# Kernel optimization log

Measured on AMD Instinct MI355X. Metric: run time of the kernel, lower is better.

## Reference

```python
import jax, jax.numpy as jnp
import numpy as np

D_LINK = 64   # link_state_dim
D_PATH = 64   # path_state_dim
T = 3
MAX_LEN = 8   # max hops per path (max(seqs)+1)
R_UNITS = 256


def _glorot(k, shape):
    lim = np.sqrt(6.0 / (shape[0] + shape[-1])).astype(np.float32)
    return jax.random.uniform(k, shape, minval=-lim, maxval=lim, dtype=jnp.float32)


def setup_inputs() -> dict:
    key = jax.random.key(0)
    ks = jax.random.split(key, 16)
    n_links, n_paths, L = 50000, 100000, MAX_LEN
    capacities = jax.random.uniform(ks[0], (n_links,), dtype=jnp.float32) + 0.5
    traffic = jax.random.uniform(ks[1], (n_paths,), dtype=jnp.float32)
    # every path traverses L links; entries sorted by path id (tf.segment_sum assumption)
    paths = jnp.repeat(jnp.arange(n_paths, dtype=jnp.int32), L)
    seqs = jnp.tile(jnp.arange(L, dtype=jnp.int32), n_paths)
    links = jax.random.randint(ks[2], (n_paths * L,), 0, n_links, dtype=jnp.int32)
    return dict(
        capacities=capacities, traffic=traffic, links=links, paths=paths, seqs=seqs,
        Wx_p=_glorot(ks[3], (D_LINK, 3 * D_PATH)), Wh_p=_glorot(ks[4], (D_PATH, 3 * D_PATH)),
        b_p=jnp.zeros((3 * D_PATH,), jnp.float32),
        Wx_e=_glorot(ks[5], (D_PATH, 3 * D_LINK)), Wh_e=_glorot(ks[6], (D_LINK, 3 * D_LINK)),
        b_e=jnp.zeros((3 * D_LINK,), jnp.float32),
        W_r1=_glorot(ks[7], (D_PATH, R_UNITS)), b_r1=jnp.zeros((R_UNITS,), jnp.float32),
        W_r2=_glorot(ks[8], (R_UNITS, R_UNITS)), b_r2=jnp.zeros((R_UNITS,), jnp.float32),
        W_f=_glorot(ks[9], (D_PATH + R_UNITS, 1)), b_f=jnp.zeros((1,), jnp.float32),
        n_links=n_links, n_paths=n_paths,
    )


def gru_cell(x, h, Wx, Wh, b):
    # Keras GRUCell (reset_after=False), gate order z, r, h
    gx = x @ Wx + b
    gh = h @ Wh
    u = h.shape[-1]
    z = jax.nn.sigmoid(gx[..., :u] + gh[..., :u])
    r = jax.nn.sigmoid(gx[..., u:2 * u] + gh[..., u:2 * u])
    hc = jnp.tanh(gx[..., 2 * u:] + r * gh[..., 2 * u:])
    return z * h + (1.0 - z) * hc


def routenet_fwd(capacities, traffic, links, paths, seqs,
                 Wx_p, Wh_p, b_p, Wx_e, Wh_e, b_e,
                 W_r1, b_r1, W_r2, b_r2, W_f, b_f, n_links, n_paths):
    link_state = jnp.concatenate(
        [capacities[:, None], jnp.zeros((n_links, D_LINK - 1), capacities.dtype)], axis=1)
    path_state = jnp.concatenate(
        [traffic[:, None], jnp.zeros((n_paths, D_PATH - 1), traffic.dtype)], axis=1)
    lens = jax.ops.segment_sum(jnp.ones_like(paths), paths, num_segments=n_paths)  # [P]

    for _ in range(T):
        h_ = link_state[links]                                        # [E, D_LINK]
        link_inputs = jnp.zeros((n_paths, MAX_LEN, D_LINK), h_.dtype).at[paths, seqs].set(h_)

        def step(h, inp):
            xt, t = inp
            hn = gru_cell(xt, h, Wx_p, Wh_p, b_p)
            valid = (t < lens)[:, None]
            hn = jnp.where(valid, hn, h)          # dynamic_rnn copies state past seq len
            out = jnp.where(valid, hn, 0.0)       # and emits zeros there
            return hn, out

        path_state, outs = jax.lax.scan(
            step, path_state,
            (jnp.transpose(link_inputs, (1, 0, 2)), jnp.arange(MAX_LEN)))
        m = jnp.transpose(outs, (1, 0, 2))[paths, seqs]               # [E, D_PATH]
        m = jax.ops.segment_sum(m, links, num_segments=n_links)      # [n_links, D_PATH]
        link_state = gru_cell(m, link_state, Wx_e, Wh_e, b_e)

    r = jax.nn.selu(path_state @ W_r1 + b_r1)
    r = jax.nn.selu(r @ W_r2 + b_r2)          # dropout inactive (training=False)
    o = jnp.concatenate([r, path_state], axis=1) @ W_f + b_f
    return o


def reference(capacities, traffic, links, paths, seqs,
              Wx_p, Wh_p, b_p, Wx_e, Wh_e, b_e,
              W_r1, b_r1, W_r2, b_r2, W_f, b_f, n_links, n_paths):
    return routenet_fwd(capacities, traffic, links, paths, seqs,
                        Wx_p, Wh_p, b_p, Wx_e, Wh_e, b_e,
                        W_r1, b_r1, W_r2, b_r2, W_f, b_f, n_links, n_paths)
```

## Files before the change

kernel.cpp:

```cpp
#include <hip/hip_runtime.h>

typedef unsigned short ushort_t;
typedef unsigned int   uint_t;
typedef short bf16x8 __attribute__((ext_vector_type(8)));
typedef float f32x4  __attribute__((ext_vector_type(4)));

#define MFMA16(a,b,c) __builtin_amdgcn_mfma_f32_16x16x32_bf16((a),(b),(c),0,0,0)

static __device__ __forceinline__ float bf2f(ushort_t b) {
  union { uint_t u; float f; } v; v.u = ((uint_t)b) << 16; return v.f;
}
static __device__ __forceinline__ ushort_t f2bf(float f) {
  union { float f; uint_t u; } v; v.f = f;
  uint_t r = v.u + 0x7fffu + ((v.u >> 16) & 1u);
  return (ushort_t)(r >> 16);
}
static __device__ __forceinline__ float frcp(float x) { return __builtin_amdgcn_rcpf(x); }
static __device__ __forceinline__ float sigm(float x) { return frcp(1.0f + __expf(-x)); }
static __device__ __forceinline__ float ftanh(float x) { return 1.0f - 2.0f * frcp(1.0f + __expf(2.0f * x)); }
static __device__ __forceinline__ float selu_f(float x) {
  float e = 1.6732632423543772f * (__expf(x) - 1.0f);
  return 1.0507009873554805f * (x > 0.0f ? x : e);
}
static __device__ __forceinline__ bf16x8 pack8(float4 a, float4 b) {
  bf16x8 r;
  r[0] = (short)f2bf(a.x); r[1] = (short)f2bf(a.y); r[2] = (short)f2bf(a.z); r[3] = (short)f2bf(a.w);
  r[4] = (short)f2bf(b.x); r[5] = (short)f2bf(b.y); r[6] = (short)f2bf(b.z); r[7] = (short)f2bf(b.w);
  return r;
}
static __device__ __forceinline__ void split8(float4 a, float4 b, bf16x8& hi, bf16x8& lo) {
  hi = pack8(a, b);
  float4 ra, rb;
  ra.x = a.x - bf2f((ushort_t)hi[0]); ra.y = a.y - bf2f((ushort_t)hi[1]);
  ra.z = a.z - bf2f((ushort_t)hi[2]); ra.w = a.w - bf2f((ushort_t)hi[3]);
  rb.x = b.x - bf2f((ushort_t)hi[4]); rb.y = b.y - bf2f((ushort_t)hi[5]);
  rb.z = b.z - bf2f((ushort_t)hi[6]); rb.w = b.w - bf2f((ushort_t)hi[7]);
  lo = pack8(ra, rb);
}

#define GFRAG(ptr, f) (*(const bf16x8*)&(ptr)[(((f) * 64 + lane)) * 8])
#define LFRAG(arr, f) (*(const bf16x8*)&(arr)[(((f) * 64 + lane)) * 8])

__global__ void detect_dtype(const uint_t* __restrict__ caps, int* __restrict__ flag) {
  int lane = threadIdx.x;
  uint_t d = caps[lane];
  uint_t lo = d & 0xFFFFu, hi = d >> 16;
  bool isbf = (lo >= 0x3F00u && lo <= 0x3FC0u) && (hi >= 0x3F00u && hi <= 0x3FC0u);
  unsigned long long m = __ballot(isbf);
  if (lane == 0) *flag = (__popcll(m) >= 48) ? 1 : 0;
}

#define NARR 14
struct ConvDesc {
  const void* src[NARR];
  float*      dst[NARR];
  int         n[NARR];
  int         blk0[NARR + 1];
};
__global__ void conv_all(ConvDesc d, const int* __restrict__ flag) {
  int isbf = *flag;
  int b = blockIdx.x;
  int a = 0;
  while (a + 1 < NARR && b >= d.blk0[a + 1]) ++a;
  int idx = (b - d.blk0[a]) * 256 + threadIdx.x;
  if (idx >= d.n[a]) return;
  d.dst[a][idx] = isbf ? bf2f(((const ushort_t*)d.src[a])[idx])
                       : ((const float*)d.src[a])[idx];
}

__global__ void pack_split(const float* __restrict__ srcA, const float* __restrict__ srcB,
                           int srcN, int colOff, int splitK, int nCk, int NT,
                           ushort_t* __restrict__ dstH, ushort_t* __restrict__ dstL) {
  int i = blockIdx.x * 256 + threadIdx.x;
  int total = nCk * NT * 512;
  if (i >= total) return;
  int j = i & 7;
  int lane = (i >> 3) & 63;
  int f = i >> 9;
  int c = f / NT, nt = f - c * NT;
  int k = c * 32 + ((lane >> 4) << 3) + j;
  int n = colOff + nt * 16 + (lane & 15);
  float v = (k < splitK) ? srcA[k * srcN + n] : srcB[(k - splitK) * srcN + n];
  ushort_t hi = f2bf(v);
  dstH[i] = hi;
  dstL[i] = f2bf(v - bf2f(hi));
}

__global__ void init_states(const float* __restrict__ caps, const float* __restrict__ traffic,
                            ushort_t* __restrict__ linkHL,
                            float* __restrict__ path_state, int n_links, int n_paths) {
  long i = (long)blockIdx.x * 256 + threadIdx.x;
  long total = (long)(n_links + n_paths) * 64;
  if (i >= total) return;
  int row = (int)(i >> 6), col = (int)(i & 63);
  if (row < n_links) {
    float v = (col == 0) ? caps[row] : 0.0f;
    ushort_t hi = f2bf(v);
    linkHL[(long)row * 128 + col] = hi;
    linkHL[(long)row * 128 + 64 + col] = f2bf(v - bf2f(hi));
  } else {
    int pr = row - n_links;
    path_state[(long)pr * 64 + col] = (col == 0) ? traffic[pr] : 0.0f;
  }
}

__global__ void hist_k(const int* __restrict__ links, int* __restrict__ cnt, int E) {
  int e = blockIdx.x * 256 + threadIdx.x;
  if (e < E) atomicAdd(&cnt[links[e]], 1);
}
__global__ void scan_k(const int* __restrict__ cnt, int* __restrict__ base,
                       int* __restrict__ cursor, int n) {
  __shared__ int part[256];
  int tid = threadIdx.x;
  int chunk = (n + 255) / 256;
  int lo = tid * chunk, hiEnd = lo + chunk; if (hiEnd > n) hiEnd = n;
  int s = 0;
  for (int i = lo; i < hiEnd; ++i) s += cnt[i];
  part[tid] = s;
  __syncthreads();
  if (tid == 0) { int acc = 0; for (int i = 0; i < 256; ++i) { int v = part[i]; part[i] = acc; acc += v; } }
  __syncthreads();
  int acc = part[tid];
  for (int i = lo; i < hiEnd; ++i) { base[i] = acc; cursor[i] = acc; acc += cnt[i]; }
}
__global__ void fill_k(const int* __restrict__ links, int* __restrict__ cursor,
                       int* __restrict__ csr, int E) {
  int e = blockIdx.x * 256 + threadIdx.x;
  if (e >= E) return;
  int pos = atomicAdd(&cursor[links[e]], 1);
  csr[pos] = e;
}

__global__ __launch_bounds__(256) void agg_kernel(
    const float* __restrict__ mF, const ushort_t* __restrict__ mH, int mmode,
    const int* __restrict__ csr, const int* __restrict__ base, const int* __restrict__ cnt,
    float* __restrict__ agg, int n_links) {
  int l = blockIdx.x * 4 + (threadIdx.x >> 6);
  if (l >= n_links) return;
  int lane = threadIdx.x & 63;
  int s = base[l], d = cnt[l];
  float acc = 0.0f;
  if (mmode == 0) {
    for (int i = 0; i < d; ++i) acc += mF[(long)csr[s + i] * 64 + lane];
  } else {
    for (int i = 0; i < d; ++i) acc += bf2f(mH[(long)csr[s + i] * 64 + lane]);
  }
  agg[(long)l * 64 + lane] = acc;
}

#define PW 10
__global__ __launch_bounds__(640) void path_kernel(
    const int* __restrict__ links,
    const ushort_t* __restrict__ linkHL,
    float* __restrict__ path_state,
    float* __restrict__ mF, ushort_t* __restrict__ mH, int mmode, float* __restrict__ agg,
    const ushort_t* __restrict__ wzrH, const ushort_t* __restrict__ wzrL,
    const ushort_t* __restrict__ wcH,  const ushort_t* __restrict__ wcL,
    const float* __restrict__ bp, const int* __restrict__ flagp) {
  __shared__ __align__(16) ushort_t s_wzr[2][32 * 512];
  __shared__ __align__(16) ushort_t s_wc[2][16 * 512];
  __shared__ __align__(16) ushort_t s_hh[PW][16][72];
  __shared__ __align__(16) ushort_t s_hl[PW][16][72];
  __shared__ float s_bias[192];

  int tid = threadIdx.x;
  int wlo = (flagp[0] == 0) ? 1 : 0;
  {
    uint_t* s0 = (uint_t*)s_wzr[0]; const uint_t* g0 = (const uint_t*)wzrH;
    for (int i = tid; i < 8192; i += 640) s0[i] = g0[i];
    uint_t* s1 = (uint_t*)s_wc[0];  const uint_t* g1 = (const uint_t*)wcH;
    for (int i = tid; i < 4096; i += 640) s1[i] = g1[i];
    if (wlo) {
      uint_t* s2 = (uint_t*)s_wzr[1]; const uint_t* g2 = (const uint_t*)wzrL;
      for (int i = tid; i < 8192; i += 640) s2[i] = g2[i];
      uint_t* s3 = (uint_t*)s_wc[1];  const uint_t* g3 = (const uint_t*)wcL;
      for (int i = tid; i < 4096; i += 640) s3[i] = g3[i];
    }
    for (int i = tid; i < 192; i += 640) s_bias[i] = bp[i];
  }

  int wv = tid >> 6, lane = tid & 63, l15 = lane & 15, quad = lane >> 4;
  int p0 = (blockIdx.x * PW + wv) * 16;

  float h[4][4];
#pragma unroll
  for (int tt = 0; tt < 4; ++tt)
#pragma unroll
    for (int r = 0; r < 4; ++r) {
      float v = path_state[(long)(p0 + quad * 4 + r) * 64 + tt * 16 + l15];
      h[tt][r] = v;
      ushort_t hi = f2bf(v);
      s_hh[wv][quad * 4 + r][tt * 16 + l15] = hi;
      s_hl[wv][quad * 4 + r][tt * 16 + l15] = f2bf(v - bf2f(hi));
    }
  __syncthreads();

  for (int t = 0; t < 8; ++t) {
    int la = links[(p0 + l15) * 8 + t];
    const ushort_t* xr = linkHL + (long)la * 128;
    bf16x8 axH0 = *(const bf16x8*)(xr + quad * 8);
    bf16x8 axH1 = *(const bf16x8*)(xr + 32 + quad * 8);
    bf16x8 axL0 = *(const bf16x8*)(xr + 64 + quad * 8);
    bf16x8 axL1 = *(const bf16x8*)(xr + 96 + quad * 8);
    bf16x8 ahH0 = *(const bf16x8*)&s_hh[wv][l15][quad * 8];
    bf16x8 ahH1 = *(const bf16x8*)&s_hh[wv][l15][32 + quad * 8];
    bf16x8 ahL0 = *(const bf16x8*)&s_hl[wv][l15][quad * 8];
    bf16x8 ahL1 = *(const bf16x8*)&s_hl[wv][l15][32 + quad * 8];

    f32x4 azr[8];
#pragma unroll
    for (int nt = 0; nt < 8; ++nt) {
      f32x4 acc = {0.f, 0.f, 0.f, 0.f};
      acc = MFMA16(axH0, LFRAG(s_wzr[0], nt), acc);
      acc = MFMA16(axH1, LFRAG(s_wzr[0], 8 + nt), acc);
      acc = MFMA16(ahH0, LFRAG(s_wzr[0], 16 + nt), acc);
      acc = MFMA16(ahH1, LFRAG(s_wzr[0], 24 + nt), acc);
      acc = MFMA16(axL0, LFRAG(s_wzr[0], nt), acc);
      acc = MFMA16(axL1, LFRAG(s_wzr[0], 8 + nt), acc);
      acc = MFMA16(ahL0, LFRAG(s_wzr[0], 16 + nt), acc);
      acc = MFMA16(ahL1, LFRAG(s_wzr[0], 24 + nt), acc);
      azr[nt] = acc;
    }
    f32x4 axc[4], ahc[4];
#pragma unroll
    for (int nt = 0; nt < 4; ++nt) {
      f32x4 a = {0.f, 0.f, 0.f, 0.f};
      a = MFMA16(axH0, LFRAG(s_wc[0], nt), a);
      a = MFMA16(axH1, LFRAG(s_wc[0], 4 + nt), a);
      a = MFMA16(axL0, LFRAG(s_wc[0], nt), a);
      a = MFMA16(axL1, LFRAG(s_wc[0], 4 + nt), a);
      axc[nt] = a;
      f32x4 b = {0.f, 0.f, 0.f, 0.f};
      b = MFMA16(ahH0, LFRAG(s_wc[0], 8 + nt), b);
      b = MFMA16(ahH1, LFRAG(s_wc[0], 12 + nt), b);
      b = MFMA16(ahL0, LFRAG(s_wc[0], 8 + nt), b);
      b = MFMA16(ahL1, LFRAG(s_wc[0], 12 + nt), b);
      ahc[nt] = b;
    }
    if (wlo) {
#pragma unroll
      for (int nt = 0; nt < 8; ++nt) {
        azr[nt] = MFMA16(axH0, LFRAG(s_wzr[1], nt), azr[nt]);
        azr[nt] = MFMA16(axH1, LFRAG(s_wzr[1], 8 + nt), azr[nt]);
        azr[nt] = MFMA16(ahH0, LFRAG(s_wzr[1], 16 + nt), azr[nt]);
        azr[nt] = MFMA16(ahH1, LFRAG(s_wzr[1], 24 + nt), azr[nt]);
      }
#pragma unroll
      for (int nt = 0; nt < 4; ++nt) {
        axc[nt] = MFMA16(axH0, LFRAG(s_wc[1], nt), axc[nt]);
        axc[nt] = MFMA16(axH1, LFRAG(s_wc[1], 4 + nt), axc[nt]);
        ahc[nt] = MFMA16(ahH0, LFRAG(s_wc[1], 8 + nt), ahc[nt]);
        ahc[nt] = MFMA16(ahH1, LFRAG(s_wc[1], 12 + nt), ahc[nt]);
      }
    }

    int lr[4] = {0, 0, 0, 0};
    if (mmode == 2) {
#pragma unroll
      for (int r = 0; r < 4; ++r) lr[r] = links[(p0 + quad * 4 + r) * 8 + t];
    }

#pragma unroll
    for (int tt = 0; tt < 4; ++tt) {
      int col = tt * 16 + l15;
      float bz = s_bias[col], br = s_bias[64 + col], bc = s_bias[128 + col];
#pragma unroll
      for (int r = 0; r < 4; ++r) {
        float z   = sigm(azr[tt][r] + bz);
        float rr  = sigm(azr[4 + tt][r] + br);
        float hcv = ftanh(axc[tt][r] + bc + rr * ahc[tt][r]);
        float hn  = z * h[tt][r] + (1.0f - z) * hcv;
        h[tt][r] = hn;
        long e = (long)(p0 + quad * 4 + r) * 8 + t;
        if (mmode == 0)      mF[e * 64 + col] = hn;
        else if (mmode == 1) mH[e * 64 + col] = f2bf(hn);
        else atomicAdd(&agg[(long)lr[r] * 64 + col], hn);
        ushort_t hi = f2bf(hn);
        s_hh[wv][quad * 4 + r][col] = hi;
        s_hl[wv][quad * 4 + r][col] = f2bf(hn - bf2f(hi));
      }
    }
  }

#pragma unroll
  for (int tt = 0; tt < 4; ++tt)
#pragma unroll
    for (int r = 0; r < 4; ++r)
      path_state[(long)(p0 + quad * 4 + r) * 64 + tt * 16 + l15] = h[tt][r];
}

__global__ __launch_bounds__(320) void link_kernel(
    const float* __restrict__ agg,
    ushort_t* __restrict__ linkHL,
    const ushort_t* __restrict__ wzrH, const ushort_t* __restrict__ wzrL,
    const ushort_t* __restrict__ wcH,  const ushort_t* __restrict__ wcL,
    const float* __restrict__ be, const int* __restrict__ flagp) {
  __shared__ __align__(16) ushort_t s_wzr[2][32 * 512];
  __shared__ __align__(16) ushort_t s_wc[2][16 * 512];
  __shared__ float s_bias[192];

  int tid = threadIdx.x;
  int wlo = (flagp[0] == 0) ? 1 : 0;
  {
    uint_t* s0 = (uint_t*)s_wzr[0]; const uint_t* g0 = (const uint_t*)wzrH;
    for (int i = tid; i < 8192; i += 320) s0[i] = g0[i];
    uint_t* s1 = (uint_t*)s_wc[0];  const uint_t* g1 = (const uint_t*)wcH;
    for (int i = tid; i < 4096; i += 320) s1[i] = g1[i];
    if (wlo) {
      uint_t* s2 = (uint_t*)s_wzr[1]; const uint_t* g2 = (const uint_t*)wzrL;
      for (int i = tid; i < 8192; i += 320) s2[i] = g2[i];
      uint_t* s3 = (uint_t*)s_wc[1];  const uint_t* g3 = (const uint_t*)wcL;
      for (int i = tid; i < 4096; i += 320) s3[i] = g3[i];
    }
    for (int i = tid; i < 192; i += 320) s_bias[i] = be[i];
  }
  __syncthreads();

  int wv = tid >> 6, lane = tid & 63, l15 = lane & 15, quad = lane >> 4;
  int l0 = (blockIdx.x * 5 + wv) * 16;

  const float* arow = agg + (long)(l0 + l15) * 64;
  float4 f0 = *(const float4*)(arow + quad * 8);
  float4 f1 = *(const float4*)(arow + quad * 8 + 4);
  float4 f2 = *(const float4*)(arow + 32 + quad * 8);
  float4 f3 = *(const float4*)(arow + 36 + quad * 8);
  bf16x8 axH0, axL0, axH1, axL1;
  split8(f0, f1, axH0, axL0);
  split8(f2, f3, axH1, axL1);
  const ushort_t* hr = linkHL + (long)(l0 + l15) * 128;
  bf16x8 ahH0 = *(const bf16x8*)(hr + quad * 8);
  bf16x8 ahH1 = *(const bf16x8*)(hr + 32 + quad * 8);
  bf16x8 ahL0 = *(const bf16x8*)(hr + 64 + quad * 8);
  bf16x8 ahL1 = *(const bf16x8*)(hr + 96 + quad * 8);

  float h[4][4];
#pragma unroll
  for (int tt = 0; tt < 4; ++tt)
#pragma unroll
    for (int r = 0; r < 4; ++r) {
      long row = (long)(l0 + quad * 4 + r) * 128;
      int col = tt * 16 + l15;
      h[tt][r] = bf2f(linkHL[row + col]) + bf2f(linkHL[row + 64 + col]);
    }

  f32x4 azr[8];
#pragma unroll
  for (int nt = 0; nt < 8; ++nt) {
    f32x4 acc = {0.f, 0.f, 0.f, 0.f};
    acc = MFMA16(axH0, LFRAG(s_wzr[0], nt), acc);
    acc = MFMA16(axH1, LFRAG(s_wzr[0], 8 + nt), acc);
    acc = MFMA16(ahH0, LFRAG(s_wzr[0], 16 + nt), acc);
    acc = MFMA16(ahH1, LFRAG(s_wzr[0], 24 + nt), acc);
    acc = MFMA16(axL0, LFRAG(s_wzr[0], nt), acc);
    acc = MFMA16(axL1, LFRAG(s_wzr[0], 8 + nt), acc);
    acc = MFMA16(ahL0, LFRAG(s_wzr[0], 16 + nt), acc);
    acc = MFMA16(ahL1, LFRAG(s_wzr[0], 24 + nt), acc);
    azr[nt] = acc;
  }
  f32x4 axc[4], ahc[4];
#pragma unroll
  for (int nt = 0; nt < 4; ++nt) {
    f32x4 a = {0.f, 0.f, 0.f, 0.f};
    a = MFMA16(axH0, LFRAG(s_wc[0], nt), a);
    a = MFMA16(axH1, LFRAG(s_wc[0], 4 + nt), a);
    a = MFMA16(axL0, LFRAG(s_wc[0], nt), a);
    a = MFMA16(axL1, LFRAG(s_wc[0], 4 + nt), a);
    axc[nt] = a;
    f32x4 b = {0.f, 0.f, 0.f, 0.f};
    b = MFMA16(ahH0, LFRAG(s_wc[0], 8 + nt), b);
    b = MFMA16(ahH1, LFRAG(s_wc[0], 12 + nt), b);
    b = MFMA16(ahL0, LFRAG(s_wc[0], 8 + nt), b);
    b = MFMA16(ahL1, LFRAG(s_wc[0], 12 + nt), b);
    ahc[nt] = b;
  }
  if (wlo) {
#pragma unroll
    for (int nt = 0; nt < 8; ++nt) {
      azr[nt] = MFMA16(axH0, LFRAG(s_wzr[1], nt), azr[nt]);
      azr[nt] = MFMA16(axH1, LFRAG(s_wzr[1], 8 + nt), azr[nt]);
      azr[nt] = MFMA16(ahH0, LFRAG(s_wzr[1], 16 + nt), azr[nt]);
      azr[nt] = MFMA16(ahH1, LFRAG(s_wzr[1], 24 + nt), azr[nt]);
    }
#pragma unroll
    for (int nt = 0; nt < 4; ++nt) {
      axc[nt] = MFMA16(axH0, LFRAG(s_wc[1], nt), axc[nt]);
      axc[nt] = MFMA16(axH1, LFRAG(s_wc[1], 4 + nt), axc[nt]);
      ahc[nt] = MFMA16(ahH0, LFRAG(s_wc[1], 8 + nt), ahc[nt]);
      ahc[nt] = MFMA16(ahH1, LFRAG(s_wc[1], 12 + nt), ahc[nt]);
    }
  }

#pragma unroll
  for (int tt = 0; tt < 4; ++tt) {
    int col = tt * 16 + l15;
    float bz = s_bias[col], br = s_bias[64 + col], bc = s_bias[128 + col];
#pragma unroll
    for (int r = 0; r < 4; ++r) {
      float z   = sigm(azr[tt][r] + bz);
      float rr  = sigm(azr[4 + tt][r] + br);
      float hcv = ftanh(axc[tt][r] + bc + rr * ahc[tt][r]);
      float hn  = z * h[tt][r] + (1.0f - z) * hcv;
      long row = (long)(l0 + quad * 4 + r) * 128;
      ushort_t hi = f2bf(hn);
      linkHL[row + col] = hi;
      linkHL[row + 64 + col] = f2bf(hn - bf2f(hi));
    }
  }
}

#define RW 8
__global__ __launch_bounds__(512) void readout_kernel(
    const float* __restrict__ path_state, int n_paths,
    const ushort_t* __restrict__ wr1H, const ushort_t* __restrict__ wr1L,
    const ushort_t* __restrict__ wr2H, const ushort_t* __restrict__ wr2L,
    const float* __restrict__ br1, const float* __restrict__ br2,
    const float* __restrict__ Wf, const float* __restrict__ bfp,
    void* __restrict__ outp, const int* __restrict__ flagp) {
  __shared__ __align__(16) ushort_t s_r1h[RW][16][264];
  __shared__ __align__(16) ushort_t s_r1l[RW][16][264];
  int tid = threadIdx.x;
  int wv = tid >> 6, lane = tid & 63, l15 = lane & 15, quad = lane >> 4;
  int p0 = (blockIdx.x * RW + wv) * 16;
  if (p0 >= n_paths) return;
  int isbf = flagp[0];
  int wlo = (isbf == 0) ? 1 : 0;

  const float* prow = path_state + (long)(p0 + l15) * 64;
  float4 g0 = *(const float4*)(prow + quad * 8);
  float4 g1 = *(const float4*)(prow + quad * 8 + 4);
  float4 g2 = *(const float4*)(prow + 32 + quad * 8);
  float4 g3 = *(const float4*)(prow + 36 + quad * 8);
  bf16x8 axH0, axL0, axH1, axL1;
  split8(g0, g1, axH0, axL0);
  split8(g2, g3, axH1, axL1);

  f32x4 a1[16];
#pragma unroll
  for (int nt = 0; nt < 16; ++nt) {
    f32x4 acc = {0.f, 0.f, 0.f, 0.f};
    acc = MFMA16(axH0, GFRAG(wr1H, nt), acc);
    acc = MFMA16(axH1, GFRAG(wr1H, 16 + nt), acc);
    acc = MFMA16(axL0, GFRAG(wr1H, nt), acc);
    acc = MFMA16(axL1, GFRAG(wr1H, 16 + nt), acc);
    a1[nt] = acc;
  }
  if (wlo) {
#pragma unroll
    for (int nt = 0; nt < 16; ++nt) {
      a1[nt] = MFMA16(axH0, GFRAG(wr1L, nt), a1[nt]);
      a1[nt] = MFMA16(axH1, GFRAG(wr1L, 16 + nt), a1[nt]);
    }
  }
#pragma unroll
  for (int tt = 0; tt < 16; ++tt) {
    float bb = br1[tt * 16 + l15];
#pragma unroll
    for (int r = 0; r < 4; ++r) {
      float v = selu_f(a1[tt][r] + bb);
      ushort_t hi = f2bf(v);
      s_r1h[wv][quad * 4 + r][tt * 16 + l15] = hi;
      s_r1l[wv][quad * 4 + r][tt * 16 + l15] = f2bf(v - bf2f(hi));
    }
  }

  f32x4 a2[16];
  f32x4 zero = {0.f, 0.f, 0.f, 0.f};
#pragma unroll
  for (int nt = 0; nt < 16; ++nt) a2[nt] = zero;
#pragma unroll
  for (int c = 0; c < 8; ++c) {
    bf16x8 afH = *(const bf16x8*)&s_r1h[wv][l15][c * 32 + quad * 8];
    bf16x8 afL = *(const bf16x8*)&s_r1l[wv][l15][c * 32 + quad * 8];
#pragma unroll
    for (int nt = 0; nt < 16; ++nt) {
      a2[nt] = MFMA16(afH, GFRAG(wr2H, c * 16 + nt), a2[nt]);
      a2[nt] = MFMA16(afL, GFRAG(wr2H, c * 16 + nt), a2[nt]);
    }
    if (wlo) {
#pragma unroll
      for (int nt = 0; nt < 16; ++nt)
        a2[nt] = MFMA16(afH, GFRAG(wr2L, c * 16 + nt), a2[nt]);
    }
  }

  float part[4] = {0.f, 0.f, 0.f, 0.f};
#pragma unroll
  for (int tt = 0; tt < 16; ++tt) {
    float wf = Wf[tt * 16 + l15];
    float bb = br2[tt * 16 + l15];
#pragma unroll
    for (int r = 0; r < 4; ++r) part[r] += selu_f(a2[tt][r] + bb) * wf;
  }
  float wfh0 = Wf[256 + l15 * 4 + 0];
  float wfh1 = Wf[256 + l15 * 4 + 1];
  float wfh2 = Wf[256 + l15 * 4 + 2];
  float wfh3 = Wf[256 + l15 * 4 + 3];
#pragma unroll
  for (int r = 0; r < 4; ++r) {
    const float4 hh = *(const float4*)&path_state[(long)(p0 + quad * 4 + r) * 64 + l15 * 4];
    part[r] += hh.x * wfh0 + hh.y * wfh1 + hh.z * wfh2 + hh.w * wfh3;
  }
#pragma unroll
  for (int msk = 1; msk < 16; msk <<= 1)
#pragma unroll
    for (int r = 0; r < 4; ++r) part[r] += __shfl_xor(part[r], msk, 64);
  if (l15 == 0) {
    float bfv = bfp[0];
    if (isbf) {
#pragma unroll
      for (int r = 0; r < 4; ++r) ((ushort_t*)outp)[p0 + quad * 4 + r] = f2bf(part[r] + bfv);
    } else {
#pragma unroll
      for (int r = 0; r < 4; ++r) ((float*)outp)[p0 + quad * 4 + r] = part[r] + bfv;
    }
  }
}

extern "C" void kernel_launch(void* const* d_in, const int* in_sizes, int n_in,
                              void* d_out, int out_size, void* d_ws, size_t ws_size,
                              hipStream_t stream) {
  const int n_links = in_sizes[0];
  const int n_paths = in_sizes[1];
  const int E       = in_sizes[2];

  char* w = (char*)d_ws;
  size_t off = 0;
  auto take = [&](size_t bytes) { size_t o = off; off += (bytes + 255) & ~(size_t)255; return o; };
  float*    path_state = (float*)(w + take((size_t)n_paths * 64 * 4));
  float*    agg        = (float*)(w + take((size_t)n_links * 64 * 4));
  ushort_t* linkHL     = (ushort_t*)(w + take((size_t)n_links * 128 * 2));
  int*      flag       = (int*)(w + take(256));
  ushort_t* wzrH_p = (ushort_t*)(w + take(32768));
  ushort_t* wzrL_p = (ushort_t*)(w + take(32768));
  ushort_t* wcH_p  = (ushort_t*)(w + take(16384));
  ushort_t* wcL_p  = (ushort_t*)(w + take(16384));
  ushort_t* wzrH_e = (ushort_t*)(w + take(32768));
  ushort_t* wzrL_e = (ushort_t*)(w + take(32768));
  ushort_t* wcH_e  = (ushort_t*)(w + take(16384));
  ushort_t* wcL_e  = (ushort_t*)(w + take(16384));
  ushort_t* wr1H   = (ushort_t*)(w + take(32768));
  ushort_t* wr1L   = (ushort_t*)(w + take(32768));
  ushort_t* wr2H   = (ushort_t*)(w + take(131072));
  ushort_t* wr2L   = (ushort_t*)(w + take(131072));
  float* c_caps    = (float*)(w + take((size_t)in_sizes[0] * 4));
  float* c_traffic = (float*)(w + take((size_t)in_sizes[1] * 4));
  float* c_Wx_p = (float*)(w + take((size_t)in_sizes[5] * 4));
  float* c_Wh_p = (float*)(w + take((size_t)in_sizes[6] * 4));
  float* c_b_p  = (float*)(w + take((size_t)in_sizes[7] * 4));
  float* c_Wx_e = (float*)(w + take((size_t)in_sizes[8] * 4));
  float* c_Wh_e = (float*)(w + take((size_t)in_sizes[9] * 4));
  float* c_b_e  = (float*)(w + take((size_t)in_sizes[10] * 4));
  float* c_Wr1  = (float*)(w + take((size_t)in_sizes[11] * 4));
  float* c_br1  = (float*)(w + take((size_t)in_sizes[12] * 4));
  float* c_Wr2  = (float*)(w + take((size_t)in_sizes[13] * 4));
  float* c_br2  = (float*)(w + take((size_t)in_sizes[14] * 4));
  float* c_Wf   = (float*)(w + take((size_t)in_sizes[15] * 4));
  float* c_bf   = (float*)(w + take((size_t)in_sizes[16] * 4));
  int* cnt    = (int*)(w + take((size_t)n_links * 4));
  int* base   = (int*)(w + take((size_t)n_links * 4));
  int* cursor = (int*)(w + take((size_t)n_links * 4));
  int* csr    = (int*)(w + take((size_t)E * 4));

  size_t rem = (ws_size > off) ? (ws_size - off) : 0;
  int mmode;
  float*    mF = nullptr;
  ushort_t* mH = nullptr;
  if (rem >= (size_t)E * 64 * 4 + 256) { mmode = 0; mF = (float*)(w + take((size_t)E * 64 * 4)); }
  else if (rem >= (size_t)E * 64 * 2 + 256) { mmode = 1; mH = (ushort_t*)(w + take((size_t)E * 64 * 2)); }
  else mmode = 2;

  detect_dtype<<<1, 64, 0, stream>>>((const uint_t*)d_in[0], flag);

  ConvDesc cd;
  float* dsts[NARR] = {c_caps, c_traffic, c_Wx_p, c_Wh_p, c_b_p, c_Wx_e, c_Wh_e, c_b_e,
                       c_Wr1, c_br1, c_Wr2, c_br2, c_Wf, c_bf};
  int    srcs[NARR] = {0, 1, 5, 6, 7, 8, 9, 10, 11, 12, 13, 14, 15, 16};
  int nblk = 0;
  for (int a = 0; a < NARR; ++a) {
    cd.src[a] = d_in[srcs[a]];
    cd.dst[a] = dsts[a];
    cd.n[a] = in_sizes[srcs[a]];
    cd.blk0[a] = nblk;
    nblk += (cd.n[a] + 255) / 256;
  }
  cd.blk0[NARR] = nblk;
  conv_all<<<nblk, 256, 0, stream>>>(cd, flag);

  {
    long total = (long)(n_links + n_paths) * 64;
    int blocks = (int)((total + 255) / 256);
    init_states<<<blocks, 256, 0, stream>>>(c_caps, c_traffic, linkHL, path_state,
                                            n_links, n_paths);
  }
  pack_split<<<64, 256, 0, stream>>>(c_Wx_p, c_Wh_p, 192, 0, 64, 4, 8, wzrH_p, wzrL_p);
  pack_split<<<16, 256, 0, stream>>>(c_Wx_p, c_Wx_p, 192, 128, 64, 2, 4, wcH_p, wcL_p);
  pack_split<<<16, 256, 0, stream>>>(c_Wh_p, c_Wh_p, 192, 128, 64, 2, 4, wcH_p + 4096, wcL_p + 4096);
  pack_split<<<64, 256, 0, stream>>>(c_Wx_e, c_Wh_e, 192, 0, 64, 4, 8, wzrH_e, wzrL_e);
  pack_split<<<16, 256, 0, stream>>>(c_Wx_e, c_Wx_e, 192, 128, 64, 2, 4, wcH_e, wcL_e);
  pack_split<<<16, 256, 0, stream>>>(c_Wh_e, c_Wh_e, 192, 128, 64, 2, 4, wcH_e + 4096, wcL_e + 4096);
  pack_split<<<64, 256, 0, stream>>>(c_Wr1, c_Wr1, 256, 0, 64, 2, 16, wr1H, wr1L);
  pack_split<<<256, 256, 0, stream>>>(c_Wr2, c_Wr2, 256, 0, 256, 8, 16, wr2H, wr2L);

  const int* links = (const int*)d_in[2];
  if (mmode < 2) {
    (void)hipMemsetAsync(cnt, 0, (size_t)n_links * 4, stream);
    hist_k<<<(E + 255) / 256, 256, 0, stream>>>(links, cnt, E);
    scan_k<<<1, 256, 0, stream>>>(cnt, base, cursor, n_links);
    fill_k<<<(E + 255) / 256, 256, 0, stream>>>(links, cursor, csr, E);
  }

  for (int it = 0; it < 3; ++it) {
    if (mmode == 2) (void)hipMemsetAsync(agg, 0, (size_t)n_links * 64 * 4, stream);
    path_kernel<<<n_paths / 160, 640, 0, stream>>>(links, linkHL, path_state,
                                                   mF, mH, mmode, agg,
                                                   wzrH_p, wzrL_p, wcH_p, wcL_p, c_b_p, flag);
    if (it < 2) {
      if (mmode < 2)
        agg_kernel<<<(n_links + 3) / 4, 256, 0, stream>>>(mF, mH, mmode, csr, base, cnt,
                                                          agg, n_links);
      link_kernel<<<n_links / 80, 320, 0, stream>>>(agg, linkHL,
                                                    wzrH_e, wzrL_e, wcH_e, wcL_e, c_b_e, flag);
    }
  }
  readout_kernel<<<(n_paths + 16 * RW - 1) / (16 * RW), 512, 0, stream>>>(
      path_state, n_paths, wr1H, wr1L, wr2H, wr2L,
      c_br1, c_br2, c_Wf, c_bf, d_out, flag);
}
```

Baseline: 1.255 ms.

## Scatter path messages directly to CSR order and split path kernel by dtype

The path kernel now writes each step's message to its link-sorted position (pos_of from fill_k), so agg_kernel reads contiguous rows instead of gathering through a csr index. On the last iteration messages are no longer stored at all, since no link update consumes them. A separate bf16-input path kernel is added that skips the low-part weights, uses 448-thread blocks with smaller shared memory for higher occupancy, and handles a ragged tail. The eight weight-packing launches are merged into one kernel. This costs a second always-launched kernel that early-exits, plus extra code paths.

```diff
diff --git a/kernel.cpp b/kernel.cpp
--- a/kernel.cpp
+++ b/kernel.cpp
@@ -68,22 +68,29 @@
                        : ((const float*)d.src[a])[idx];
 }
 
-__global__ void pack_split(const float* __restrict__ srcA, const float* __restrict__ srcB,
-                           int srcN, int colOff, int splitK, int nCk, int NT,
-                           ushort_t* __restrict__ dstH, ushort_t* __restrict__ dstL) {
-  int i = blockIdx.x * 256 + threadIdx.x;
-  int total = nCk * NT * 512;
-  if (i >= total) return;
+struct PackAll {
+  const float* A[8];
+  const float* B[8];
+  ushort_t* dH[8];
+  ushort_t* dL[8];
+  int srcN[8], colOff[8], splitK[8], nCk[8], NT[8], blk0[9];
+};
+__global__ void pack_all(PackAll P) {
+  int b = blockIdx.x;
+  int a = 0;
+  while (a + 1 < 8 && b >= P.blk0[a + 1]) ++a;
+  int i = (b - P.blk0[a]) * 256 + threadIdx.x;
   int j = i & 7;
   int lane = (i >> 3) & 63;
   int f = i >> 9;
-  int c = f / NT, nt = f - c * NT;
+  int c = f / P.NT[a], nt = f - c * P.NT[a];
   int k = c * 32 + ((lane >> 4) << 3) + j;
-  int n = colOff + nt * 16 + (lane & 15);
-  float v = (k < splitK) ? srcA[k * srcN + n] : srcB[(k - splitK) * srcN + n];
+  int n = P.colOff[a] + nt * 16 + (lane & 15);
+  float v = (k < P.splitK[a]) ? P.A[a][k * P.srcN[a] + n]
+                              : P.B[a][(k - P.splitK[a]) * P.srcN[a] + n];
   ushort_t hi = f2bf(v);
-  dstH[i] = hi;
-  dstL[i] = f2bf(v - bf2f(hi));
+  P.dH[a][i] = hi;
+  P.dL[a][i] = f2bf(v - bf2f(hi));
 }
 
 __global__ void init_states(const float* __restrict__ caps, const float* __restrict__ traffic,
@@ -124,16 +131,15 @@
   for (int i = lo; i < hiEnd; ++i) { base[i] = acc; cursor[i] = acc; acc += cnt[i]; }
 }
 __global__ void fill_k(const int* __restrict__ links, int* __restrict__ cursor,
-                       int* __restrict__ csr, int E) {
+                       int* __restrict__ pos_of, int E) {
   int e = blockIdx.x * 256 + threadIdx.x;
   if (e >= E) return;
-  int pos = atomicAdd(&cursor[links[e]], 1);
-  csr[pos] = e;
+  pos_of[e] = atomicAdd(&cursor[links[e]], 1);
 }
 
 __global__ __launch_bounds__(256) void agg_kernel(
     const float* __restrict__ mF, const ushort_t* __restrict__ mH, int mmode,
-    const int* __restrict__ csr, const int* __restrict__ base, const int* __restrict__ cnt,
+    const int* __restrict__ base, const int* __restrict__ cnt,
     float* __restrict__ agg, int n_links) {
   int l = blockIdx.x * 4 + (threadIdx.x >> 6);
   if (l >= n_links) return;
@@ -141,59 +147,58 @@
   int s = base[l], d = cnt[l];
   float acc = 0.0f;
   if (mmode == 0) {
-    for (int i = 0; i < d; ++i) acc += mF[(long)csr[s + i] * 64 + lane];
+    for (int i = 0; i < d; ++i) acc += mF[(long)(s + i) * 64 + lane];
   } else {
-    for (int i = 0; i < d; ++i) acc += bf2f(mH[(long)csr[s + i] * 64 + lane]);
+    for (int i = 0; i < d; ++i) acc += bf2f(mH[(long)(s + i) * 64 + lane]);
   }
   agg[(long)l * 64 + lane] = acc;
 }
 
-#define PW 10
-__global__ __launch_bounds__(640) void path_kernel(
+#define PWB 7
+__global__ __launch_bounds__(448, 3) void path_kernel_bf16(
     const int* __restrict__ links,
     const ushort_t* __restrict__ linkHL,
     float* __restrict__ path_state,
-    float* __restrict__ mF, ushort_t* __restrict__ mH, int mmode, float* __restrict__ agg,
-    const ushort_t* __restrict__ wzrH, const ushort_t* __restrict__ wzrL,
-    const ushort_t* __restrict__ wcH,  const ushort_t* __restrict__ wcL,
-    const float* __restrict__ bp, const int* __restrict__ flagp) {
-  __shared__ __align__(16) ushort_t s_wzr[2][32 * 512];
-  __shared__ __align__(16) ushort_t s_wc[2][16 * 512];
-  __shared__ __align__(16) ushort_t s_hh[PW][16][72];
-  __shared__ __align__(16) ushort_t s_hl[PW][16][72];
+    float* __restrict__ mF, ushort_t* __restrict__ mH, int mmode, int store_m,
+    const int* __restrict__ pos_of, float* __restrict__ agg,
+    const ushort_t* __restrict__ wzrH, const ushort_t* __restrict__ wcH,
+    const float* __restrict__ bp, const int* __restrict__ flagp, int n_paths) {
+  __shared__ __align__(16) ushort_t s_wzr[32 * 512];
+  __shared__ __align__(16) ushort_t s_wc[16 * 512];
+  __shared__ __align__(16) ushort_t s_hh[PWB][16][68];
+  __shared__ __align__(16) ushort_t s_hl[PWB][16][68];
   __shared__ float s_bias[192];
 
+  if (flagp[0] == 0) return;
+
   int tid = threadIdx.x;
-  int wlo = (flagp[0] == 0) ? 1 : 0;
   {
-    uint_t* s0 = (uint_t*)s_wzr[0]; const uint_t* g0 = (const uint_t*)wzrH;
-    for (int i = tid; i < 8192; i += 640) s0[i] = g0[i];
-    uint_t* s1 = (uint_t*)s_wc[0];  const uint_t* g1 = (const uint_t*)wcH;
-    for (int i = tid; i < 4096; i += 640) s1[i] = g1[i];
-    if (wlo) {
-      uint_t* s2 = (uint_t*)s_wzr[1]; const uint_t* g2 = (const uint_t*)wzrL;
-      for (int i = tid; i < 8192; i += 640) s2[i] = g2[i];
-      uint_t* s3 = (uint_t*)s_wc[1];  const uint_t* g3 = (const uint_t*)wcL;
-      for (int i = tid; i < 4096; i += 640) s3[i] = g3[i];
-    }
-    for (int i = tid; i < 192; i += 640) s_bias[i] = bp[i];
+    uint_t* s0 = (uint_t*)s_wzr; const uint_t* g0 = (const uint_t*)wzrH;
+    for (int i = tid; i < 8192; i += 448) s0[i] = g0[i];
+    uint_t* s1 = (uint_t*)s_wc;  const uint_t* g1 = (const uint_t*)wcH;
+    for (int i = tid; i < 4096; i += 448) s1[i] = g1[i];
+    for (int i = tid; i < 192; i += 448) s_bias[i] = bp[i];
   }
 
   int wv = tid >> 6, lane = tid & 63, l15 = lane & 15, quad = lane >> 4;
-  int p0 = (blockIdx.x * PW + wv) * 16;
+  int p0 = (blockIdx.x * PWB + wv) * 16;
+  bool valid = (p0 < n_paths);
 
   float h[4][4];
-#pragma unroll
-  for (int tt = 0; tt < 4; ++tt)
-#pragma unroll
-    for (int r = 0; r < 4; ++r) {
-      float v = path_state[(long)(p0 + quad * 4 + r) * 64 + tt * 16 + l15];
-      h[tt][r] = v;
-      ushort_t hi = f2bf(v);
-      s_hh[wv][quad * 4 + r][tt * 16 + l15] = hi;
-      s_hl[wv][quad * 4 + r][tt * 16 + l15] = f2bf(v - bf2f(hi));
-    }
+  if (valid) {
+#pragma unroll
+    for (int tt = 0; tt < 4; ++tt)
+#pragma unroll
+      for (int r = 0; r < 4; ++r) {
+        float v = path_state[(long)(p0 + quad * 4 + r) * 64 + tt * 16 + l15];
+        h[tt][r] = v;
+        ushort_t hi = f2bf(v);
+        s_hh[wv][quad * 4 + r][tt * 16 + l15] = hi;
+        s_hl[wv][quad * 4 + r][tt * 16 + l15] = f2bf(v - bf2f(hi));
+      }
+  }
   __syncthreads();
+  if (!valid) return;
 
   for (int t = 0; t < 8; ++t) {
     int la = links[(p0 + l15) * 8 + t];
@@ -211,6 +216,137 @@
 #pragma unroll
     for (int nt = 0; nt < 8; ++nt) {
       f32x4 acc = {0.f, 0.f, 0.f, 0.f};
+      acc = MFMA16(axH0, LFRAG(s_wzr, nt), acc);
+      acc = MFMA16(axH1, LFRAG(s_wzr, 8 + nt), acc);
+      acc = MFMA16(ahH0, LFRAG(s_wzr, 16 + nt), acc);
+      acc = MFMA16(ahH1, LFRAG(s_wzr, 24 + nt), acc);
+      acc = MFMA16(axL0, LFRAG(s_wzr, nt), acc);
+      acc = MFMA16(axL1, LFRAG(s_wzr, 8 + nt), acc);
+      acc = MFMA16(ahL0, LFRAG(s_wzr, 16 + nt), acc);
+      acc = MFMA16(ahL1, LFRAG(s_wzr, 24 + nt), acc);
+      azr[nt] = acc;
+    }
+    f32x4 axc[4], ahc[4];
+#pragma unroll
+    for (int nt = 0; nt < 4; ++nt) {
+      f32x4 a = {0.f, 0.f, 0.f, 0.f};
+      a = MFMA16(axH0, LFRAG(s_wc, nt), a);
+      a = MFMA16(axH1, LFRAG(s_wc, 4 + nt), a);
+      a = MFMA16(axL0, LFRAG(s_wc, nt), a);
+      a = MFMA16(axL1, LFRAG(s_wc, 4 + nt), a);
+      axc[nt] = a;
+      f32x4 b = {0.f, 0.f, 0.f, 0.f};
+      b = MFMA16(ahH0, LFRAG(s_wc, 8 + nt), b);
+      b = MFMA16(ahH1, LFRAG(s_wc, 12 + nt), b);
+      b = MFMA16(ahL0, LFRAG(s_wc, 8 + nt), b);
+      b = MFMA16(ahL1, LFRAG(s_wc, 12 + nt), b);
+      ahc[nt] = b;
+    }
+
+    int pr[4] = {0, 0, 0, 0};
+    if (store_m) {
+      if (mmode == 2) {
+#pragma unroll
+        for (int r = 0; r < 4; ++r) pr[r] = links[(p0 + quad * 4 + r) * 8 + t];
+      } else {
+#pragma unroll
+        for (int r = 0; r < 4; ++r) pr[r] = pos_of[(p0 + quad * 4 + r) * 8 + t];
+      }
+    }
+
+#pragma unroll
+    for (int tt = 0; tt < 4; ++tt) {
+      int col = tt * 16 + l15;
+      float bz = s_bias[col], br = s_bias[64 + col], bc = s_bias[128 + col];
+#pragma unroll
+      for (int r = 0; r < 4; ++r) {
+        float z   = sigm(azr[tt][r] + bz);
+        float rr  = sigm(azr[4 + tt][r] + br);
+        float hcv = ftanh(axc[tt][r] + bc + rr * ahc[tt][r]);
+        float hn  = z * h[tt][r] + (1.0f - z) * hcv;
+        h[tt][r] = hn;
+        if (store_m) {
+          if (mmode == 0)      mF[(long)pr[r] * 64 + col] = hn;
+          else if (mmode == 1) mH[(long)pr[r] * 64 + col] = f2bf(hn);
+          else atomicAdd(&agg[(long)pr[r] * 64 + col], hn);
+        }
+        ushort_t hi = f2bf(hn);
+        s_hh[wv][quad * 4 + r][col] = hi;
+        s_hl[wv][quad * 4 + r][col] = f2bf(hn - bf2f(hi));
+      }
+    }
+  }
+
+#pragma unroll
+  for (int tt = 0; tt < 4; ++tt)
+#pragma unroll
+    for (int r = 0; r < 4; ++r)
+      path_state[(long)(p0 + quad * 4 + r) * 64 + tt * 16 + l15] = h[tt][r];
+}
+
+#define PW 10
+__global__ __launch_bounds__(640) void path_kernel_f32(
+    const int* __restrict__ links,
+    const ushort_t* __restrict__ linkHL,
+    float* __restrict__ path_state,
+    float* __restrict__ mF, ushort_t* __restrict__ mH, int mmode, int store_m,
+    const int* __restrict__ pos_of, float* __restrict__ agg,
+    const ushort_t* __restrict__ wzrH, const ushort_t* __restrict__ wzrL,
+    const ushort_t* __restrict__ wcH,  const ushort_t* __restrict__ wcL,
+    const float* __restrict__ bp, const int* __restrict__ flagp) {
+  __shared__ __align__(16) ushort_t s_wzr[2][32 * 512];
+  __shared__ __align__(16) ushort_t s_wc[2][16 * 512];
+  __shared__ __align__(16) ushort_t s_hh[PW][16][72];
+  __shared__ __align__(16) ushort_t s_hl[PW][16][72];
+  __shared__ float s_bias[192];
+
+  if (flagp[0] != 0) return;
+
+  int tid = threadIdx.x;
+  {
+    uint_t* s0 = (uint_t*)s_wzr[0]; const uint_t* g0 = (const uint_t*)wzrH;
+    for (int i = tid; i < 8192; i += 640) s0[i] = g0[i];
+    uint_t* s1 = (uint_t*)s_wc[0];  const uint_t* g1 = (const uint_t*)wcH;
+    for (int i = tid; i < 4096; i += 640) s1[i] = g1[i];
+    uint_t* s2 = (uint_t*)s_wzr[1]; const uint_t* g2 = (const uint_t*)wzrL;
+    for (int i = tid; i < 8192; i += 640) s2[i] = g2[i];
+    uint_t* s3 = (uint_t*)s_wc[1];  const uint_t* g3 = (const uint_t*)wcL;
+    for (int i = tid; i < 4096; i += 640) s3[i] = g3[i];
+    for (int i = tid; i < 192; i += 640) s_bias[i] = bp[i];
+  }
+
+  int wv = tid >> 6, lane = tid & 63, l15 = lane & 15, quad = lane >> 4;
+  int p0 = (blockIdx.x * PW + wv) * 16;
+
+  float h[4][4];
+#pragma unroll
+  for (int tt = 0; tt < 4; ++tt)
+#pragma unroll
+    for (int r = 0; r < 4; ++r) {
+      float v = path_state[(long)(p0 + quad * 4 + r) * 64 + tt * 16 + l15];
+      h[tt][r] = v;
+      ushort_t hi = f2bf(v);
+      s_hh[wv][quad * 4 + r][tt * 16 + l15] = hi;
+      s_hl[wv][quad * 4 + r][tt * 16 + l15] = f2bf(v - bf2f(hi));
+    }
+  __syncthreads();
+
+  for (int t = 0; t < 8; ++t) {
+    int la = links[(p0 + l15) * 8 + t];
+    const ushort_t* xr = linkHL + (long)la * 128;
+    bf16x8 axH0 = *(const bf16x8*)(xr + quad * 8);
+    bf16x8 axH1 = *(const bf16x8*)(xr + 32 + quad * 8);
+    bf16x8 axL0 = *(const bf16x8*)(xr + 64 + quad * 8);
+    bf16x8 axL1 = *(const bf16x8*)(xr + 96 + quad * 8);
+    bf16x8 ahH0 = *(const bf16x8*)&s_hh[wv][l15][quad * 8];
+    bf16x8 ahH1 = *(const bf16x8*)&s_hh[wv][l15][32 + quad * 8];
+    bf16x8 ahL0 = *(const bf16x8*)&s_hl[wv][l15][quad * 8];
+    bf16x8 ahL1 = *(const bf16x8*)&s_hl[wv][l15][32 + quad * 8];
+
+    f32x4 azr[8];
+#pragma unroll
+    for (int nt = 0; nt < 8; ++nt) {
+      f32x4 acc = {0.f, 0.f, 0.f, 0.f};
       acc = MFMA16(axH0, LFRAG(s_wzr[0], nt), acc);
       acc = MFMA16(axH1, LFRAG(s_wzr[0], 8 + nt), acc);
       acc = MFMA16(ahH0, LFRAG(s_wzr[0], 16 + nt), acc);
@@ -219,6 +355,10 @@
       acc = MFMA16(axL1, LFRAG(s_wzr[0], 8 + nt), acc);
       acc = MFMA16(ahL0, LFRAG(s_wzr[0], 16 + nt), acc);
       acc = MFMA16(ahL1, LFRAG(s_wzr[0], 24 + nt), acc);
+      acc = MFMA16(axH0, LFRAG(s_wzr[1], nt), acc);
+      acc = MFMA16(axH1, LFRAG(s_wzr[1], 8 + nt), acc);
+      acc = MFMA16(ahH0, LFRAG(s_wzr[1], 16 + nt), acc);
+      acc = MFMA16(ahH1, LFRAG(s_wzr[1], 24 + nt), acc);
       azr[nt] = acc;
     }
     f32x4 axc[4], ahc[4];
@@ -229,35 +369,28 @@
       a = MFMA16(axH1, LFRAG(s_wc[0], 4 + nt), a);
       a = MFMA16(axL0, LFRAG(s_wc[0], nt), a);
       a = MFMA16(axL1, LFRAG(s_wc[0], 4 + nt), a);
+      a = MFMA16(axH0, LFRAG(s_wc[1], nt), a);
+      a = MFMA16(axH1, LFRAG(s_wc[1], 4 + nt), a);
       axc[nt] = a;
       f32x4 b = {0.f, 0.f, 0.f, 0.f};
       b = MFMA16(ahH0, LFRAG(s_wc[0], 8 + nt), b);
       b = MFMA16(ahH1, LFRAG(s_wc[0], 12 + nt), b);
       b = MFMA16(ahL0, LFRAG(s_wc[0], 8 + nt), b);
       b = MFMA16(ahL1, LFRAG(s_wc[0], 12 + nt), b);
+      b = MFMA16(ahH0, LFRAG(s_wc[1], 8 + nt), b);
+      b = MFMA16(ahH1, LFRAG(s_wc[1], 12 + nt), b);
       ahc[nt] = b;
     }
-    if (wlo) {
-#pragma unroll
-      for (int nt = 0; nt < 8; ++nt) {
-        azr[nt] = MFMA16(axH0, LFRAG(s_wzr[1], nt), azr[nt]);
-        azr[nt] = MFMA16(axH1, LFRAG(s_wzr[1], 8 + nt), azr[nt]);
-        azr[nt] = MFMA16(ahH0, LFRAG(s_wzr[1], 16 + nt), azr[nt]);
-        azr[nt] = MFMA16(ahH1, LFRAG(s_wzr[1], 24 + nt), azr[nt]);
+
+    int pr[4] = {0, 0, 0, 0};
+    if (store_m) {
+      if (mmode == 2) {
+#pragma unroll
+        for (int r = 0; r < 4; ++r) pr[r] = links[(p0 + quad * 4 + r) * 8 + t];
+      } else {
+#pragma unroll
+        for (int r = 0; r < 4; ++r) pr[r] = pos_of[(p0 + quad * 4 + r) * 8 + t];
       }
-#pragma unroll
-      for (int nt = 0; nt < 4; ++nt) {
-        axc[nt] = MFMA16(axH0, LFRAG(s_wc[1], nt), axc[nt]);
-        axc[nt] = MFMA16(axH1, LFRAG(s_wc[1], 4 + nt), axc[nt]);
-        ahc[nt] = MFMA16(ahH0, LFRAG(s_wc[1], 8 + nt), ahc[nt]);
-        ahc[nt] = MFMA16(ahH1, LFRAG(s_wc[1], 12 + nt), ahc[nt]);
-      }
-    }
-
-    int lr[4] = {0, 0, 0, 0};
-    if (mmode == 2) {
-#pragma unroll
-      for (int r = 0; r < 4; ++r) lr[r] = links[(p0 + quad * 4 + r) * 8 + t];
     }
 
 #pragma unroll
@@ -271,10 +404,11 @@
         float hcv = ftanh(axc[tt][r] + bc + rr * ahc[tt][r]);
         float hn  = z * h[tt][r] + (1.0f - z) * hcv;
         h[tt][r] = hn;
-        long e = (long)(p0 + quad * 4 + r) * 8 + t;
-        if (mmode == 0)      mF[e * 64 + col] = hn;
-        else if (mmode == 1) mH[e * 64 + col] = f2bf(hn);
-        else atomicAdd(&agg[(long)lr[r] * 64 + col], hn);
+        if (store_m) {
+          if (mmode == 0)      mF[(long)pr[r] * 64 + col] = hn;
+          else if (mmode == 1) mH[(long)pr[r] * 64 + col] = f2bf(hn);
+          else atomicAdd(&agg[(long)pr[r] * 64 + col], hn);
+        }
         ushort_t hi = f2bf(hn);
         s_hh[wv][quad * 4 + r][col] = hi;
         s_hl[wv][quad * 4 + r][col] = f2bf(hn - bf2f(hi));
@@ -559,7 +693,7 @@
   int* cnt    = (int*)(w + take((size_t)n_links * 4));
   int* base   = (int*)(w + take((size_t)n_links * 4));
   int* cursor = (int*)(w + take((size_t)n_links * 4));
-  int* csr    = (int*)(w + take((size_t)E * 4));
+  int* pos_of = (int*)(w + take((size_t)E * 4));
 
   size_t rem = (ws_size > off) ? (ws_size - off) : 0;
   int mmode;
@@ -592,31 +726,49 @@
     init_states<<<blocks, 256, 0, stream>>>(c_caps, c_traffic, linkHL, path_state,
                                             n_links, n_paths);
   }
-  pack_split<<<64, 256, 0, stream>>>(c_Wx_p, c_Wh_p, 192, 0, 64, 4, 8, wzrH_p, wzrL_p);
-  pack_split<<<16, 256, 0, stream>>>(c_Wx_p, c_Wx_p, 192, 128, 64, 2, 4, wcH_p, wcL_p);
-  pack_split<<<16, 256, 0, stream>>>(c_Wh_p, c_Wh_p, 192, 128, 64, 2, 4, wcH_p + 4096, wcL_p + 4096);
-  pack_split<<<64, 256, 0, stream>>>(c_Wx_e, c_Wh_e, 192, 0, 64, 4, 8, wzrH_e, wzrL_e);
-  pack_split<<<16, 256, 0, stream>>>(c_Wx_e, c_Wx_e, 192, 128, 64, 2, 4, wcH_e, wcL_e);
-  pack_split<<<16, 256, 0, stream>>>(c_Wh_e, c_Wh_e, 192, 128, 64, 2, 4, wcH_e + 4096, wcL_e + 4096);
-  pack_split<<<64, 256, 0, stream>>>(c_Wr1, c_Wr1, 256, 0, 64, 2, 16, wr1H, wr1L);
-  pack_split<<<256, 256, 0, stream>>>(c_Wr2, c_Wr2, 256, 0, 256, 8, 16, wr2H, wr2L);
+  {
+    PackAll P;
+    const float* As[8] = {c_Wx_p, c_Wx_p, c_Wh_p, c_Wx_e, c_Wx_e, c_Wh_e, c_Wr1, c_Wr2};
+    const float* Bs[8] = {c_Wh_p, c_Wx_p, c_Wh_p, c_Wh_e, c_Wx_e, c_Wh_e, c_Wr1, c_Wr2};
+    ushort_t* dH[8] = {wzrH_p, wcH_p, wcH_p + 4096, wzrH_e, wcH_e, wcH_e + 4096, wr1H, wr2H};
+    ushort_t* dL[8] = {wzrL_p, wcL_p, wcL_p + 4096, wzrL_e, wcL_e, wcL_e + 4096, wr1L, wr2L};
+    int srcN[8]   = {192, 192, 192, 192, 192, 192, 256, 256};
+    int colOff[8] = {0, 128, 128, 0, 128, 128, 0, 0};
+    int splitK[8] = {64, 64, 64, 64, 64, 64, 64, 256};
+    int nCk[8]    = {4, 2, 2, 4, 2, 2, 2, 8};
+    int NT[8]     = {8, 4, 4, 8, 4, 4, 16, 16};
+    int pb = 0;
+    for (int a = 0; a < 8; ++a) {
+      P.A[a] = As[a]; P.B[a] = Bs[a]; P.dH[a] = dH[a]; P.dL[a] = dL[a];
+      P.srcN[a] = srcN[a]; P.colOff[a] = colOff[a]; P.splitK[a] = splitK[a];
+      P.nCk[a] = nCk[a]; P.NT[a] = NT[a]; P.blk0[a] = pb;
+      pb += nCk[a] * NT[a] * 2;
+    }
+    P.blk0[8] = pb;
+    pack_all<<<pb, 256, 0, stream>>>(P);
+  }
 
   const int* links = (const int*)d_in[2];
   if (mmode < 2) {
     (void)hipMemsetAsync(cnt, 0, (size_t)n_links * 4, stream);
     hist_k<<<(E + 255) / 256, 256, 0, stream>>>(links, cnt, E);
     scan_k<<<1, 256, 0, stream>>>(cnt, base, cursor, n_links);
-    fill_k<<<(E + 255) / 256, 256, 0, stream>>>(links, cursor, csr, E);
-  }
-
+    fill_k<<<(E + 255) / 256, 256, 0, stream>>>(links, cursor, pos_of, E);
+  }
+
+  int grid_bf = (n_paths + 16 * PWB - 1) / (16 * PWB);
   for (int it = 0; it < 3; ++it) {
-    if (mmode == 2) (void)hipMemsetAsync(agg, 0, (size_t)n_links * 64 * 4, stream);
-    path_kernel<<<n_paths / 160, 640, 0, stream>>>(links, linkHL, path_state,
-                                                   mF, mH, mmode, agg,
-                                                   wzrH_p, wzrL_p, wcH_p, wcL_p, c_b_p, flag);
+    int store_m = (it < 2) ? 1 : 0;
+    if (mmode == 2 && store_m) (void)hipMemsetAsync(agg, 0, (size_t)n_links * 64 * 4, stream);
+    path_kernel_bf16<<<grid_bf, 16 * PWB * 4, 0, stream>>>(
+        links, linkHL, path_state, mF, mH, mmode, store_m, pos_of, agg,
+        wzrH_p, wcH_p, c_b_p, flag, n_paths);
+    path_kernel_f32<<<n_paths / 160, 640, 0, stream>>>(
+        links, linkHL, path_state, mF, mH, mmode, store_m, pos_of, agg,
+        wzrH_p, wzrL_p, wcH_p, wcL_p, c_b_p, flag);
     if (it < 2) {
       if (mmode < 2)
-        agg_kernel<<<(n_links + 3) / 4, 256, 0, stream>>>(mF, mH, mmode, csr, base, cnt,
+        agg_kernel<<<(n_links + 3) / 4, 256, 0, stream>>>(mF, mH, mmode, base, cnt,
                                                           agg, n_links);
       link_kernel<<<n_links / 80, 320, 0, stream>>>(agg, linkHL,
                                                     wzrH_e, wzrL_e, wcH_e, wcL_e, c_b_e, flag);
```

Result: faster. 1.196 ms (-4.7%).
